# Kernel tuning notes

Measured on AMD Instinct MI355X. Metric: run time of the kernel, lower is better.

## Reference

```python
import jax, jax.numpy as jnp
import numpy as np

B, S, D, H = 4, 2048, 1024, 16
DK = D // H
THETA = 10000.0


def apply_rope(x, pos, theta):
    # x: [B, H, S, DK], pos: [S] int
    d = x.shape[-1]
    inv_freq = theta ** (-jnp.arange(0, d, 2, dtype=jnp.float32) / d)  # [d/2]
    ang = pos.astype(jnp.float32)[:, None] * inv_freq[None, :]          # [S, d/2]
    cos, sin = jnp.cos(ang), jnp.sin(ang)
    x1 = x[..., 0::2]
    x2 = x[..., 1::2]
    r1 = x1 * cos - x2 * sin
    r2 = x1 * sin + x2 * cos
    return jnp.stack([r1, r2], axis=-1).reshape(x.shape)


def setup_inputs() -> dict:
    key = jax.random.key(0)
    ks = jax.random.split(key, 5)
    scale = 1.0 / np.sqrt(D)
    x = jax.random.normal(ks[0], (B, S, D), dtype=jnp.float32)
    Wq = jax.random.normal(ks[1], (D, D), dtype=jnp.float32) * scale
    Wk = jax.random.normal(ks[2], (D, D), dtype=jnp.float32) * scale
    Wv = jax.random.normal(ks[3], (D, D), dtype=jnp.float32) * scale
    Wo = jax.random.normal(ks[4], (D, D), dtype=jnp.float32) * scale
    token_positions = jnp.arange(S, dtype=jnp.int32)
    return {"x": x, "token_positions": token_positions,
            "Wq": Wq, "Wk": Wk, "Wv": Wv, "Wo": Wo}


def reference(x, token_positions, Wq, Wk, Wv, Wo):
    b, s, d = x.shape
    # Linear (no bias), weight stored [out, in]: y = x @ W.T
    q = (x @ Wq.T).reshape(b, s, H, DK).transpose(0, 2, 1, 3)  # [B,H,S,DK]
    k = (x @ Wk.T).reshape(b, s, H, DK).transpose(0, 2, 1, 3)
    v = (x @ Wv.T).reshape(b, s, H, DK).transpose(0, 2, 1, 3)
    q = apply_rope(q, token_positions, THETA)
    k = apply_rope(k, token_positions, THETA)
    scores = jnp.einsum('bhqd,bhkd->bhqk', q, k) / jnp.sqrt(jnp.float32(DK))
    causal = jnp.tril(jnp.ones((s, s), dtype=bool))
    scores = jnp.where(causal, scores, -jnp.inf)
    attn = jax.nn.softmax(scores, axis=-1)
    out = jnp.einsum('bhqk,bhkd->bhqd', attn, v)
    out = out.transpose(0, 2, 1, 3).reshape(b, s, d)
    return out @ Wo.T
```

## Files before the change

kernel.cpp:

```cpp
#include <hip/hip_runtime.h>

typedef unsigned short u16;
typedef __bf16 bf16x8 __attribute__((ext_vector_type(8)));
typedef float f32x4 __attribute__((ext_vector_type(4)));
typedef u16 u16x8 __attribute__((ext_vector_type(8)));
typedef u16 u16x4 __attribute__((ext_vector_type(4)));
typedef short s16x4 __attribute__((ext_vector_type(4)));

union V8 { u16x8 u; bf16x8 b; };
union V4 { u16x4 u; s16x4 s; unsigned w[2]; };

#define NB 4
#define NS 2048
#define ND 1024
#define NH 16
#define NDK 64
#define LP 80
#define CP 136
#define QSCL 0.18033688011112042f
#define FMAX 20.0f

__device__ __forceinline__ u16 f2bf(float f) {
  union { float f; unsigned u; } v; v.f = f;
  return (u16)((v.u + 0x7fffu + ((v.u >> 16) & 1u)) >> 16);
}

__device__ __forceinline__ unsigned pk2bf(float a, float b) {
#if __has_builtin(__builtin_amdgcn_cvt_pk_bf16_f32)
  auto v = __builtin_amdgcn_cvt_pk_bf16_f32(a, b);
  unsigned r; __builtin_memcpy(&r, &v, 4);
  return r;
#else
  return (unsigned)f2bf(a) | ((unsigned)f2bf(b) << 16);
#endif
}

__device__ __forceinline__ float fexp2(float x) {
#if __has_builtin(__builtin_amdgcn_exp2f)
  return __builtin_amdgcn_exp2f(x);
#else
  return exp2f(x);
#endif
}

__device__ __forceinline__ bf16x8 lds_frag(const u16* p) {
  V8 t; t.u = *(const u16x8*)p; return t.b;
}

__device__ __forceinline__ void gld16(const u16* g, u16* l) {
  __builtin_amdgcn_global_load_lds(
      (const __attribute__((address_space(1))) void*)g,
      (__attribute__((address_space(3))) void*)l, 16, 0, 0);
}

__global__ __launch_bounds__(256) void cvt_bf16(const float* __restrict__ s,
                                                u16* __restrict__ d, int n) {
  const int i = (blockIdx.x * 256 + threadIdx.x) * 8;
  if (i >= n) return;
  const f32x4 lo = *(const f32x4*)(s + i);
  const f32x4 hi = *(const f32x4*)(s + i + 4);
  union { unsigned w[4]; u16x8 v; } o;
  o.w[0] = pk2bf(lo[0], lo[1]);
  o.w[1] = pk2bf(lo[2], lo[3]);
  o.w[2] = pk2bf(hi[0], hi[1]);
  o.w[3] = pk2bf(hi[2], hi[3]);
  *(u16x8*)(d + i) = o.v;
}

__global__ __launch_bounds__(256) void cvt_w4(const float* __restrict__ w0,
                                              const float* __restrict__ w1,
                                              const float* __restrict__ w2,
                                              const float* __restrict__ w3,
                                              u16* __restrict__ d) {
  const float* s = (blockIdx.y == 0) ? w0 : (blockIdx.y == 1) ? w1
                 : (blockIdx.y == 2) ? w2 : w3;
  const int i = (blockIdx.x * 256 + threadIdx.x) * 8;
  const f32x4 lo = *(const f32x4*)(s + i);
  const f32x4 hi = *(const f32x4*)(s + i + 4);
  union { unsigned w[4]; u16x8 v; } o;
  o.w[0] = pk2bf(lo[0], lo[1]);
  o.w[1] = pk2bf(lo[2], lo[3]);
  o.w[2] = pk2bf(hi[0], hi[1]);
  o.w[3] = pk2bf(hi[2], hi[3]);
  *(u16x8*)(d + (size_t)blockIdx.y * ND * ND + i) = o.v;
}

__global__ __launch_bounds__(256) void gemm_qkv(
    const u16* __restrict__ X, const u16* __restrict__ W0,
    const u16* __restrict__ W1, const u16* __restrict__ W2,
    void* __restrict__ O0, void* __restrict__ O1, void* __restrict__ O2,
    const int* __restrict__ tokpos, int modebase) {
  __shared__ u16 smem[4 * 128 * 64];
  u16* A0 = smem;
  u16* B0 = smem + 128 * 64;
  u16* A1 = smem + 2 * 128 * 64;
  u16* B1 = smem + 3 * 128 * 64;
  const int tid = threadIdx.x;
  const int lane = tid & 63;
  const int w = tid >> 6;
  const int quad = lane >> 4;
  const int l15 = lane & 15;
  const int z = blockIdx.z;
  const u16* Wp = (z == 0) ? W0 : (z == 1) ? W1 : W2;
  void* Op = (z == 0) ? O0 : (z == 1) ? O1 : O2;
  const int mode = modebase + z;
  const int m0 = blockIdx.x * 128;
  const int n0 = blockIdx.y * 128;
  const int wm = (w >> 1) * 64;
  const int wn = (w & 1) * 64;

  const int lrow = lane >> 3;
  const int lcol = ((lane & 7) ^ lrow) * 8;
  const u16* Ag = X + (size_t)(m0 + w * 32 + lrow) * ND + lcol;
  const u16* Bg = Wp + (size_t)(n0 + w * 32 + lrow) * ND + lcol;
  const int wbase = w * 32;

  f32x4 acc[4][4];
  const f32x4 z4 = {0.f, 0.f, 0.f, 0.f};
  for (int i = 0; i < 4; i++)
    for (int j = 0; j < 4; j++) acc[i][j] = z4;

  auto STAGE = [&](u16* dA, u16* dB, int k0) {
    for (int i = 0; i < 4; i++) {
      gld16(Ag + (size_t)(i * 8) * ND + k0, dA + (wbase + i * 8) * 64);
      gld16(Bg + (size_t)(i * 8) * ND + k0, dB + (wbase + i * 8) * 64);
    }
  };
  auto COMPUTE = [&](const u16* A, const u16* Bm) {
    for (int kk = 0; kk < 2; kk++) {
      bf16x8 af[4], bfr[4];
      for (int mt = 0; mt < 4; mt++) {
        const int R = wm + mt * 16 + l15;
        af[mt] = lds_frag(&A[R * 64 + (((kk * 4 + quad) ^ (R & 7)) * 8)]);
      }
      for (int nt = 0; nt < 4; nt++) {
        const int R = wn + nt * 16 + l15;
        bfr[nt] = lds_frag(&Bm[R * 64 + (((kk * 4 + quad) ^ (R & 7)) * 8)]);
      }
      for (int mt = 0; mt < 4; mt++)
        for (int nt = 0; nt < 4; nt++)
          acc[mt][nt] = __builtin_amdgcn_mfma_f32_16x16x32_bf16(
              af[mt], bfr[nt], acc[mt][nt], 0, 0, 0);
    }
  };

  STAGE(A0, B0, 0);
  __syncthreads();
  for (int k0 = 0; k0 < ND; k0 += 128) {
    STAGE(A1, B1, k0 + 64);
    COMPUTE(A0, B0);
    __syncthreads();
    if (k0 + 128 < ND) STAGE(A0, B0, k0 + 128);
    COMPUTE(A1, B1);
    __syncthreads();
  }

  if (mode < 2) {
    u16* cb = smem;
    for (int nt = 0; nt < 4; nt++) {
      const int n_g = n0 + wn + nt * 16 + l15;
      const int dk = n_g & 63;
      const float sgn = (dk & 1) ? 1.f : -1.f;
      const float inv_freq = __expf(-(float)(dk >> 1) * 0.28782313662425572f);
      for (int mt = 0; mt < 4; mt++) {
        const int mrow = wm + mt * 16 + quad * 4;
        for (int r = 0; r < 4; r++) {
          const int m_g = m0 + mrow + r;
          float v = acc[mt][nt][r];
          const int s_i = m_g & (NS - 1);
          const float pos = (float)tokpos[s_i];
          const float partner = __shfl_xor(v, 1);
          float sn, cs;
          __sincosf(pos * inv_freq, &sn, &cs);
          v = v * cs + partner * sn * sgn;
          if (mode == 0) v *= QSCL;
          cb[(mrow + r) * CP + wn + nt * 16 + l15] = f2bf(v);
        }
      }
    }
    __syncthreads();
    const int c = (tid & 15) * 8;
    const int h = (n0 + c) >> 6;
    const int dk0 = (n0 + c) & 63;
    for (int p = 0; p < 8; p++) {
      const int row = p * 16 + (tid >> 4);
      const int m_g = m0 + row;
      const int b = m_g >> 11;
      const int s_i = m_g & (NS - 1);
      *(u16x8*)&((u16*)Op)[(size_t)(((b * NH) + h) * NS + s_i) * NDK + dk0] =
          *(const u16x8*)&cb[row * CP + c];
    }
  } else if (mode == 2) {
    u16* cbT = smem;
    for (int nt = 0; nt < 4; nt++)
      for (int mt = 0; mt < 4; mt++)
        for (int r = 0; r < 4; r++)
          cbT[(wn + nt * 16 + l15) * CP + wm + mt * 16 + quad * 4 + r] =
              f2bf(acc[mt][nt][r]);
    __syncthreads();
    const int b = m0 >> 11;
    const int s0 = m0 & (NS - 1);
    const int col = (tid & 15) * 8;
    for (int p = 0; p < 8; p++) {
      const int row = p * 16 + (tid >> 4);
      const int dkg = n0 + row;
      const int h = dkg >> 6;
      *(u16x8*)&((u16*)Op)[(size_t)(((b * NH) + h) * NDK + (dkg & 63)) * NS +
                           s0 + col] = *(const u16x8*)&cbT[row * CP + col];
    }
  } else {
    for (int nt = 0; nt < 4; nt++) {
      const int n_g = n0 + wn + nt * 16 + l15;
      for (int mt = 0; mt < 4; mt++) {
        const int mb = m0 + wm + mt * 16 + quad * 4;
        for (int r = 0; r < 4; r++)
          ((float*)Op)[(size_t)(mb + r) * ND + n_g] = acc[mt][nt][r];
      }
    }
  }
}

__global__ __launch_bounds__(512) void attn(const u16* __restrict__ Q,
                                            const u16* __restrict__ Kc,
                                            const u16* __restrict__ Vt,
                                            u16* __restrict__ AO,
                                            unsigned* __restrict__ ctr) {
  __shared__ u16 smem[2 * 64 * LP];
  u16* kt = smem;
  u16* vt = smem + 64 * LP;
  __shared__ unsigned s_item;
  const int tid = threadIdx.x;
  const int lane = tid & 63;
  const int w = tid >> 6;
  const int quad = lane >> 4;
  const int l15 = lane & 15;

  if (tid == 0) s_item = atomicAdd(ctr, 1u) & 1023u;
  __syncthreads();
  const unsigned item = s_item;
  const int bh = (int)(item >> 4);
  const int jj = (int)(item & 15u);
  const int qt = (jj & 1) ? (jj >> 1) : (15 - (jj >> 1));
  const int q0 = qt * 128;
  const int qg = q0 + w * 16 + l15;
  const int qmin = q0 + w * 16;

  const u16* Qb = Q + (size_t)bh * NS * NDK + (size_t)qg * NDK + quad * 8;
  const bf16x8 qf0 = lds_frag(Qb);
  const bf16x8 qf1 = lds_frag(Qb + 32);

  f32x4 oacc[4];
  const f32x4 z4 = {0.f, 0.f, 0.f, 0.f};
  for (int i = 0; i < 4; i++) oacc[i] = z4;
  float lsum = 0.f;

  const int srow = tid >> 3;
  const int sg = tid & 7;
  const u16* Kb = Kc + (size_t)bh * NS * NDK;
  const u16* Vg = Vt + (size_t)bh * NDK * NS;

  u16x8 kreg = *(const u16x8*)(Kb + (size_t)srow * NDK + sg * 8);
  u16x8 vreg = *(const u16x8*)(Vg + (size_t)srow * NS + sg * 8);

  const int jend = q0 + 64;
  const f32x4 nF = {-FMAX, -FMAX, -FMAX, -FMAX};
  for (int j0 = 0; j0 <= jend; j0 += 64) {
    __syncthreads();
    *(u16x8*)&kt[srow * LP + (sg ^ (srow & 7)) * 8] = kreg;
    *(u16x8*)&vt[srow * LP + (sg ^ (srow & 7)) * 8] = vreg;
    __syncthreads();
    if (j0 + 64 <= jend) {
      const int nj = j0 + 64;
      kreg = *(const u16x8*)(Kb + (size_t)(nj + srow) * NDK + sg * 8);
      vreg = *(const u16x8*)(Vg + (size_t)srow * NS + nj + sg * 8);
    }

    if (j0 <= qmin + 15) {
      f32x4 sa[4];
      for (int i = 0; i < 4; i++) sa[i] = nF;
      for (int kk = 0; kk < 2; kk++) {
        const bf16x8 qf = kk ? qf1 : qf0;
        for (int nt = 0; nt < 4; nt++) {
          const int row = nt * 16 + l15;
          const bf16x8 kf =
              lds_frag(&kt[row * LP + ((kk * 4 + quad) ^ (row & 7)) * 8]);
          sa[nt] = __builtin_amdgcn_mfma_f32_16x16x32_bf16(kf, qf, sa[nt], 0, 0, 0);
        }
      }

      const bool dotail = (j0 + 63 > qmin);
      float p[4][4];
      for (int nt = 0; nt < 4; nt++)
        for (int r = 0; r < 4; r++) {
          float e = fexp2(sa[nt][r]);
          if (dotail && (j0 + nt * 16 + quad * 4 + r) > qg) e = 0.f;
          p[nt][r] = e;
          lsum += e;
        }

      s16x4 pa[4];
      for (int nt = 0; nt < 4; nt++) {
        V4 t;
        t.w[0] = pk2bf(p[nt][0], p[nt][1]);
        t.w[1] = pk2bf(p[nt][2], p[nt][3]);
        pa[nt] = t.s;
      }

      for (int dt = 0; dt < 4; dt++) {
        const int dk = dt * 16 + l15;
        const int xr = dk & 7;
        for (int nt = 0; nt < 4; nt++) {
          const int chunk = 2 * nt + (quad >> 1);
          V4 t;
          t.u = *(const u16x4*)&vt[dk * LP + (chunk ^ xr) * 8 + 4 * (quad & 1)];
          oacc[dt] = __builtin_amdgcn_mfma_f32_16x16x16bf16_1k(pa[nt], t.s,
                                                               oacc[dt], 0, 0, 0);
        }
      }
    }
  }

  lsum += __shfl_xor(lsum, 16);
  lsum += __shfl_xor(lsum, 32);
  float lq[4];
  for (int r = 0; r < 4; r++) lq[r] = __shfl(lsum, quad * 4 + r);

  __syncthreads();
  u16* ob = smem;
  for (int dt = 0; dt < 4; dt++)
    for (int r = 0; r < 4; r++)
      ob[(w * 16 + quad * 4 + r) * 72 + dt * 16 + l15] =
          f2bf(oacc[dt][r] / lq[r]);
  __syncthreads();
  const int b = bh >> 4, h = bh & 15;
  for (int p2 = 0; p2 < 2; p2++) {
    const int idx = p2 * 512 + tid;
    const int row = idx >> 3;
    const int c = (idx & 7) * 8;
    *(u16x8*)&AO[(size_t)(b * NS + q0 + row) * ND + h * 64 + c] =
        *(const u16x8*)&ob[row * 72 + c];
  }
}

extern "C" void kernel_launch(void* const* d_in, const int* in_sizes, int n_in,
                              void* d_out, int out_size, void* d_ws, size_t ws_size,
                              hipStream_t stream) {
  const float* x = (const float*)d_in[0];
  const int* tp = (const int*)d_in[1];
  const float* Wq = (const float*)d_in[2];
  const float* Wk = (const float*)d_in[3];
  const float* Wv = (const float*)d_in[4];
  const float* Wo = (const float*)d_in[5];

  const size_t NE = (size_t)NB * NS * ND;
  const int NW = ND * ND;
  u16* Qb = (u16*)d_ws;
  u16* Kb = Qb + NE;
  u16* Vtb = Kb + NE;
  u16* Xbf = Vtb + NE;
  u16* Wbf = Xbf + NE;
  unsigned* ctr = (unsigned*)(Wbf + 4 * (size_t)NW);

  dim3 blk(256);
  cvt_bf16<<<dim3((unsigned)(NE / 2048)), blk, 0, stream>>>(x, Xbf, (int)NE);
  cvt_w4<<<dim3(NW / 2048, 4), blk, 0, stream>>>(Wq, Wk, Wv, Wo, Wbf);
  gemm_qkv<<<dim3(64, 8, 3), blk, 0, stream>>>(
      Xbf, Wbf, Wbf + (size_t)NW, Wbf + 2 * (size_t)NW, Qb, Kb, Vtb, tp, 0);
  attn<<<dim3(1024), dim3(512), 0, stream>>>(Qb, Kb, Vtb, Xbf, ctr);
  gemm_qkv<<<dim3(64, 8, 1), blk, 0, stream>>>(
      Xbf, Wbf + 3 * (size_t)NW, Wbf + 3 * (size_t)NW, Wbf + 3 * (size_t)NW,
      d_out, d_out, d_out, tp, 3);
}
```

Baseline: 319.2 us.

## Replace async LDS GEMM pipeline with register staging; tune attention loop scheduling

The QKV/output GEMM drops its double-buffered global_load_lds pipeline and XOR swizzle. It now loads tiles into registers, then writes them to a single padded LDS buffer (LP stride) between barriers. This removes the async-copy path but also loses the overlap between loads and compute. The attention kernel gains several changes: precomputed LDS offsets, s_setprio around the MFMA blocks, an occupancy hint of two blocks per CU, the causal masking moved out of the exp loop, and a split row-sum accumulator that adds more independent additions.

```diff
diff --git a/kernel.cpp b/kernel.cpp
--- a/kernel.cpp
+++ b/kernel.cpp
@@ -45,12 +45,6 @@
 
 __device__ __forceinline__ bf16x8 lds_frag(const u16* p) {
   V8 t; t.u = *(const u16x8*)p; return t.b;
-}
-
-__device__ __forceinline__ void gld16(const u16* g, u16* l) {
-  __builtin_amdgcn_global_load_lds(
-      (const __attribute__((address_space(1))) void*)g,
-      (__attribute__((address_space(3))) void*)l, 16, 0, 0);
 }
 
 __global__ __launch_bounds__(256) void cvt_bf16(const float* __restrict__ s,
@@ -90,11 +84,9 @@
     const u16* __restrict__ W1, const u16* __restrict__ W2,
     void* __restrict__ O0, void* __restrict__ O1, void* __restrict__ O2,
     const int* __restrict__ tokpos, int modebase) {
-  __shared__ u16 smem[4 * 128 * 64];
-  u16* A0 = smem;
-  u16* B0 = smem + 128 * 64;
-  u16* A1 = smem + 2 * 128 * 64;
-  u16* B1 = smem + 3 * 128 * 64;
+  __shared__ u16 smem[2 * 128 * LP];
+  u16* ldsA = smem;
+  u16* ldsB = smem + 128 * LP;
   const int tid = threadIdx.x;
   const int lane = tid & 63;
   const int w = tid >> 6;
@@ -109,51 +101,41 @@
   const int wm = (w >> 1) * 64;
   const int wn = (w & 1) * 64;
 
-  const int lrow = lane >> 3;
-  const int lcol = ((lane & 7) ^ lrow) * 8;
-  const u16* Ag = X + (size_t)(m0 + w * 32 + lrow) * ND + lcol;
-  const u16* Bg = Wp + (size_t)(n0 + w * 32 + lrow) * ND + lcol;
-  const int wbase = w * 32;
+  const int srow = tid >> 3;
+  const int scol = (tid & 7) * 8;
+  const u16* Ag = X + (size_t)(m0 + srow) * ND + scol;
+  const u16* Bg = Wp + (size_t)(n0 + srow) * ND + scol;
 
   f32x4 acc[4][4];
   const f32x4 z4 = {0.f, 0.f, 0.f, 0.f};
   for (int i = 0; i < 4; i++)
     for (int j = 0; j < 4; j++) acc[i][j] = z4;
 
-  auto STAGE = [&](u16* dA, u16* dB, int k0) {
-    for (int i = 0; i < 4; i++) {
-      gld16(Ag + (size_t)(i * 8) * ND + k0, dA + (wbase + i * 8) * 64);
-      gld16(Bg + (size_t)(i * 8) * ND + k0, dB + (wbase + i * 8) * 64);
-    }
-  };
-  auto COMPUTE = [&](const u16* A, const u16* Bm) {
+  for (int k0 = 0; k0 < ND; k0 += 64) {
+    u16x8 ar[4], br[4];
+    for (int r = 0; r < 4; r++) {
+      ar[r] = *(const u16x8*)(Ag + (size_t)r * 32 * ND + k0);
+      br[r] = *(const u16x8*)(Bg + (size_t)r * 32 * ND + k0);
+    }
+    __syncthreads();
+    for (int r = 0; r < 4; r++) {
+      *(u16x8*)&ldsA[(r * 32 + srow) * LP + scol] = ar[r];
+      *(u16x8*)&ldsB[(r * 32 + srow) * LP + scol] = br[r];
+    }
+    __syncthreads();
     for (int kk = 0; kk < 2; kk++) {
       bf16x8 af[4], bfr[4];
-      for (int mt = 0; mt < 4; mt++) {
-        const int R = wm + mt * 16 + l15;
-        af[mt] = lds_frag(&A[R * 64 + (((kk * 4 + quad) ^ (R & 7)) * 8)]);
-      }
-      for (int nt = 0; nt < 4; nt++) {
-        const int R = wn + nt * 16 + l15;
-        bfr[nt] = lds_frag(&Bm[R * 64 + (((kk * 4 + quad) ^ (R & 7)) * 8)]);
-      }
+      for (int mt = 0; mt < 4; mt++)
+        af[mt] = lds_frag(&ldsA[(wm + mt * 16 + l15) * LP + (kk * 4 + quad) * 8]);
+      for (int nt = 0; nt < 4; nt++)
+        bfr[nt] = lds_frag(&ldsB[(wn + nt * 16 + l15) * LP + (kk * 4 + quad) * 8]);
       for (int mt = 0; mt < 4; mt++)
         for (int nt = 0; nt < 4; nt++)
           acc[mt][nt] = __builtin_amdgcn_mfma_f32_16x16x32_bf16(
               af[mt], bfr[nt], acc[mt][nt], 0, 0, 0);
     }
-  };
-
-  STAGE(A0, B0, 0);
+  }
   __syncthreads();
-  for (int k0 = 0; k0 < ND; k0 += 128) {
-    STAGE(A1, B1, k0 + 64);
-    COMPUTE(A0, B0);
-    __syncthreads();
-    if (k0 + 128 < ND) STAGE(A0, B0, k0 + 128);
-    COMPUTE(A1, B1);
-    __syncthreads();
-  }
 
   if (mode < 2) {
     u16* cb = smem;
@@ -220,11 +202,11 @@
   }
 }
 
-__global__ __launch_bounds__(512) void attn(const u16* __restrict__ Q,
-                                            const u16* __restrict__ Kc,
-                                            const u16* __restrict__ Vt,
-                                            u16* __restrict__ AO,
-                                            unsigned* __restrict__ ctr) {
+__global__ __launch_bounds__(512, 2) void attn(const u16* __restrict__ Q,
+                                               const u16* __restrict__ Kc,
+                                               const u16* __restrict__ Vt,
+                                               u16* __restrict__ AO,
+                                               unsigned* __restrict__ ctr) {
   __shared__ u16 smem[2 * 64 * LP];
   u16* kt = smem;
   u16* vt = smem + 64 * LP;
@@ -249,13 +231,35 @@
   const bf16x8 qf0 = lds_frag(Qb);
   const bf16x8 qf1 = lds_frag(Qb + 32);
 
+  int koff[2][4];
+#pragma unroll
+  for (int kk = 0; kk < 2; kk++)
+#pragma unroll
+    for (int nt = 0; nt < 4; nt++) {
+      const int row = nt * 16 + l15;
+      koff[kk][nt] = row * LP + (((kk * 4 + quad) ^ (row & 7)) * 8);
+    }
+  int voff[4][4];
+#pragma unroll
+  for (int dt = 0; dt < 4; dt++) {
+    const int dk = dt * 16 + l15;
+    const int xr = dk & 7;
+#pragma unroll
+    for (int nt = 0; nt < 4; nt++) {
+      const int chunk = 2 * nt + (quad >> 1);
+      voff[dt][nt] = dk * LP + ((chunk ^ xr) * 8) + 4 * (quad & 1);
+    }
+  }
+
   f32x4 oacc[4];
   const f32x4 z4 = {0.f, 0.f, 0.f, 0.f};
+#pragma unroll
   for (int i = 0; i < 4; i++) oacc[i] = z4;
-  float lsum = 0.f;
+  float ls0 = 0.f, ls1 = 0.f;
 
   const int srow = tid >> 3;
   const int sg = tid & 7;
+  const int woff = srow * LP + ((sg ^ (srow & 7)) * 8);
   const u16* Kb = Kc + (size_t)bh * NS * NDK;
   const u16* Vg = Vt + (size_t)bh * NDK * NS;
 
@@ -266,8 +270,8 @@
   const f32x4 nF = {-FMAX, -FMAX, -FMAX, -FMAX};
   for (int j0 = 0; j0 <= jend; j0 += 64) {
     __syncthreads();
-    *(u16x8*)&kt[srow * LP + (sg ^ (srow & 7)) * 8] = kreg;
-    *(u16x8*)&vt[srow * LP + (sg ^ (srow & 7)) * 8] = vreg;
+    *(u16x8*)&kt[woff] = kreg;
+    *(u16x8*)&vt[woff] = vreg;
     __syncthreads();
     if (j0 + 64 <= jend) {
       const int nj = j0 + 64;
@@ -277,28 +281,43 @@
 
     if (j0 <= qmin + 15) {
       f32x4 sa[4];
+#pragma unroll
       for (int i = 0; i < 4; i++) sa[i] = nF;
+      __builtin_amdgcn_s_setprio(1);
+#pragma unroll
       for (int kk = 0; kk < 2; kk++) {
         const bf16x8 qf = kk ? qf1 : qf0;
+#pragma unroll
         for (int nt = 0; nt < 4; nt++) {
-          const int row = nt * 16 + l15;
-          const bf16x8 kf =
-              lds_frag(&kt[row * LP + ((kk * 4 + quad) ^ (row & 7)) * 8]);
+          const bf16x8 kf = lds_frag(&kt[koff[kk][nt]]);
           sa[nt] = __builtin_amdgcn_mfma_f32_16x16x32_bf16(kf, qf, sa[nt], 0, 0, 0);
         }
       }
-
-      const bool dotail = (j0 + 63 > qmin);
+      __builtin_amdgcn_s_setprio(0);
+
       float p[4][4];
+#pragma unroll
       for (int nt = 0; nt < 4; nt++)
-        for (int r = 0; r < 4; r++) {
-          float e = fexp2(sa[nt][r]);
-          if (dotail && (j0 + nt * 16 + quad * 4 + r) > qg) e = 0.f;
-          p[nt][r] = e;
-          lsum += e;
-        }
+#pragma unroll
+        for (int r = 0; r < 4; r++) p[nt][r] = fexp2(sa[nt][r]);
+      if (j0 + 63 > qmin) {
+#pragma unroll
+        for (int nt = 0; nt < 4; nt++)
+#pragma unroll
+          for (int r = 0; r < 4; r++)
+            if ((j0 + nt * 16 + quad * 4 + r) > qg) p[nt][r] = 0.f;
+      }
+      {
+        float s0 = (p[0][0] + p[0][1]) + (p[0][2] + p[0][3]);
+        float s1 = (p[1][0] + p[1][1]) + (p[1][2] + p[1][3]);
+        float s2 = (p[2][0] + p[2][1]) + (p[2][2] + p[2][3]);
+        float s3 = (p[3][0] + p[3][1]) + (p[3][2] + p[3][3]);
+        ls0 += s0 + s1;
+        ls1 += s2 + s3;
+      }
 
       s16x4 pa[4];
+#pragma unroll
       for (int nt = 0; nt < 4; nt++) {
         V4 t;
         t.w[0] = pk2bf(p[nt][0], p[nt][1]);
@@ -306,33 +325,39 @@
         pa[nt] = t.s;
       }
 
+      __builtin_amdgcn_s_setprio(1);
+#pragma unroll
       for (int dt = 0; dt < 4; dt++) {
-        const int dk = dt * 16 + l15;
-        const int xr = dk & 7;
+#pragma unroll
         for (int nt = 0; nt < 4; nt++) {
-          const int chunk = 2 * nt + (quad >> 1);
           V4 t;
-          t.u = *(const u16x4*)&vt[dk * LP + (chunk ^ xr) * 8 + 4 * (quad & 1)];
+          t.u = *(const u16x4*)&vt[voff[dt][nt]];
           oacc[dt] = __builtin_amdgcn_mfma_f32_16x16x16bf16_1k(pa[nt], t.s,
                                                                oacc[dt], 0, 0, 0);
         }
       }
-    }
-  }
-
+      __builtin_amdgcn_s_setprio(0);
+    }
+  }
+
+  float lsum = ls0 + ls1;
   lsum += __shfl_xor(lsum, 16);
   lsum += __shfl_xor(lsum, 32);
   float lq[4];
+#pragma unroll
   for (int r = 0; r < 4; r++) lq[r] = __shfl(lsum, quad * 4 + r);
 
   __syncthreads();
   u16* ob = smem;
+#pragma unroll
   for (int dt = 0; dt < 4; dt++)
+#pragma unroll
     for (int r = 0; r < 4; r++)
       ob[(w * 16 + quad * 4 + r) * 72 + dt * 16 + l15] =
           f2bf(oacc[dt][r] / lq[r]);
   __syncthreads();
   const int b = bh >> 4, h = bh & 15;
+#pragma unroll
   for (int p2 = 0; p2 < 2; p2++) {
     const int idx = p2 * 512 + tid;
     const int row = idx >> 3;
```

New measurement: 284.1 us. 1.12x faster.
